# Kernel tuning notes

Measured on AMD Instinct MI355X. Metric: run time of the kernel, lower is better.

Reference implementation:

```python
import jax, jax.numpy as jnp
import numpy as np
from jax import lax

K = 3      # kernel_size
C = 64     # n_feat
B, H, W = 2, 256, 256


def _conv(x, w, b, pad):
    # NCHW conv, stride 1
    out = lax.conv_general_dilated(x, w, (1, 1), [(pad, pad), (pad, pad)],
                                   dimension_numbers=('NCHW', 'OIHW', 'NCHW'))
    return out + b[None, :, None, None]


def _prelu(x, a):
    # nn.PReLU() with a single shared learnable slope (init 0.25)
    return jnp.where(x >= 0, x, a * x)


def setup_inputs():
    key = jax.random.key(0)
    ks = jax.random.split(key, 20)
    s = 0.05
    def w(k, shape):
        return jax.random.normal(k, shape, jnp.float32) * s
    inp = {
        'image': jax.random.normal(ks[0], (B, C, H, W), jnp.float32),
        'guidance': jax.random.normal(ks[1], (B, C, H, W), jnp.float32),
        # self.tensor: 1x1 conv (2C -> C) + PReLU (shared with jbf_conv's act)
        'tensor_w': w(ks[2], (C, 2 * C, 1, 1)),
        'tensor_b': jnp.zeros((C,), jnp.float32),
        'a_jbf': jnp.full((1,), 0.25, jnp.float32),
        'kg_w1': w(ks[3], (C, C, 3, 3)), 'kg_b1': jnp.zeros((C,), jnp.float32),
        'kg_w2': w(ks[4], (C, C, 3, 3)), 'kg_b2': jnp.zeros((C,), jnp.float32),
        'kg_w3': w(ks[5], (C, C, 3, 3)), 'kg_b3': jnp.zeros((C,), jnp.float32),
        'kg_w4': w(ks[6], (C, C, 3, 3)), 'kg_b4': jnp.zeros((C,), jnp.float32),
        'kg_w5': w(ks[7], (K * K * C, C, 1, 1)),
        'kg_b5': jnp.zeros((K * K * C,), jnp.float32),
        'a_kg': jnp.full((1,), 0.25, jnp.float32),
        # jbf_conv: 3x3 C->C, PReLU (shared a_jbf), 3x3 C->C
        'jbf_w1': w(ks[8], (C, C, 3, 3)), 'jbf_b1': jnp.zeros((C,), jnp.float32),
        'jbf_w2': w(ks[9], (C, C, 3, 3)), 'jbf_b2': jnp.zeros((C,), jnp.float32),
    }
    return inp


def reference(image, guidance, tensor_w, tensor_b, a_jbf,
              kg_w1, kg_b1, kg_w2, kg_b2, kg_w3, kg_b3, kg_w4, kg_b4,
              kg_w5, kg_b5, a_kg, jbf_w1, jbf_b1, jbf_w2, jbf_b2):
    b, c, h, w = image.shape
    # fuse target+guidance features
    t = _prelu(_conv(jnp.concatenate([image, guidance], axis=1), tensor_w, tensor_b, 0), a_jbf)
    # concat_kg: predict per-pixel dynamic kernel (b, K*K*c, h, w)
    y = t
    for wt, bs in ((kg_w1, kg_b1), (kg_w2, kg_b2), (kg_w3, kg_b3), (kg_w4, kg_b4)):
        y = _prelu(_conv(y, wt, bs, 1), a_kg)
    bi_kernel = _conv(y, kg_w5, kg_b5, 0)
    # unfold: torch layout is channel-major (c, ki, kj) along dim 1
    p = (K - 1) // 2
    xp = jnp.pad(image, ((0, 0), (0, 0), (p, p), (p, p)))
    taps = [xp[:, :, i:i + h, j:j + w] for i in range(K) for j in range(K)]
    patch = jnp.stack(taps, axis=2).reshape(b, c * K * K, h, w)
    # NOTE: faithful to source -- (c*K*K) flat layout reinterpreted as (K*K, c)
    jbf = (patch * bi_kernel).reshape(b, K * K, c, h, w).sum(axis=1)
    out = _conv(_prelu(_conv(jbf, jbf_w1, jbf_b1, 1), a_jbf), jbf_w2, jbf_b2, 1)
    return out + image
```

## Files before the change

### kernel.cpp

```cpp
#include <hip/hip_runtime.h>

#define HW 65536

typedef __bf16 bf16x8 __attribute__((ext_vector_type(8)));
typedef float f32x16 __attribute__((ext_vector_type(16)));

__device__ inline unsigned short f2bf(float x) {
    union { float f; unsigned u; } v; v.f = x;
    unsigned r = v.u + 0x7FFF + ((v.u >> 16) & 1);
    return (unsigned short)(r >> 16);
}
__device__ inline float bfhi2f(unsigned u) {
    union { unsigned u; float f; } v; v.u = u & 0xffff0000u; return v.f;
}
__device__ inline float bflo2f(unsigned u) {
    union { unsigned u; float f; } v; v.u = u << 16; return v.f;
}

union FragU { uint4 u; bf16x8 v; };
__device__ inline bf16x8 ld_frag(const uint4* p) { FragU t; t.u = *p; return t.v; }

__global__ __launch_bounds__(256) void k_wprep(
    const float* __restrict__ w0, const float* __restrict__ w1,
    const float* __restrict__ w2, const float* __restrict__ w3,
    const float* __restrict__ w4, const float* __restrict__ w5,
    const float* __restrict__ w5c, const float* __restrict__ tw,
    unsigned short* __restrict__ wT)
{
    int y = blockIdx.y;
    unsigned short* o = wT + (size_t)y * 36864;
    if (y < 6) {
        const float* ws_[6] = {w0, w1, w2, w3, w4, w5};
        const float* w = ws_[y];
        for (int e = blockIdx.x * 256 + threadIdx.x; e < 36864; e += gridDim.x * 256) {
            int tap = e >> 12, oc = (e >> 6) & 63, ic = e & 63;
            int igg = ic >> 3, j = ic & 7;
            int dst = ((tap * 8 + igg) * 64 + oc) * 8 + j;
            o[dst] = f2bf(w[(oc * 64 + ic) * 9 + tap]);
        }
    } else if (y == 6) {
        for (int e = blockIdx.x * 256 + threadIdx.x; e < 36864; e += gridDim.x * 256)
            o[e] = f2bf(w5c[e]);
    } else {
        for (int e = blockIdx.x * 256 + threadIdx.x; e < 8192; e += gridDim.x * 256) {
            int oc = e >> 7, ic = e & 127;
            int kg = ic >> 3, j = ic & 7;
            o[((kg * 64 + oc) << 3) + j] = f2bf(tw[e]);
        }
    }
}

__global__ __launch_bounds__(256) void k_tr(
    const float* __restrict__ img, const float* __restrict__ gd,
    unsigned short* __restrict__ imgT, unsigned short* __restrict__ gdT)
{
    __shared__ float sT[64 * 66];
    int tid = threadIdx.x;
    int z = blockIdx.y;
    int b = z & 1;
    const float* src = (z >> 1) ? gd : img;
    unsigned short* dst = (z >> 1) ? gdT : imgT;
    int px0 = blockIdx.x * 64;
    size_t sbase = (size_t)b * 64 * HW + px0;

#pragma unroll
    for (int i = 0; i < 4; ++i) {
        int e = i * 256 + tid;
        int ic = e >> 4, seg = e & 15;
        float4 v = *(const float4*)(src + sbase + (size_t)ic * HW + seg * 4);
        float* p = &sT[ic * 66 + seg * 4];
        ((float2*)p)[0] = make_float2(v.x, v.y);
        ((float2*)p)[1] = make_float2(v.z, v.w);
    }
    __syncthreads();

    size_t dbase = (size_t)b * HW * 64 + (size_t)px0 * 64;
#pragma unroll
    for (int k = 0; k < 2; ++k) {
        int idx = k * 256 + tid;
        int px = idx >> 3, u = idx & 7;
        union { uint4 q; unsigned short h[8]; } o;
#pragma unroll
        for (int j = 0; j < 8; ++j)
            o.h[j] = f2bf(sT[(u * 8 + j) * 66 + px]);
        *(uint4*)(dst + dbase + (size_t)px * 64 + u * 8) = o.q;
    }
}

__global__ __launch_bounds__(256, 4) void k_fusem(
    const unsigned short* __restrict__ imgT, const unsigned short* __restrict__ gdT,
    const unsigned short* __restrict__ wTf, const float* __restrict__ bias,
    const float* __restrict__ a, unsigned short* __restrict__ out)
{
    __shared__ __align__(16) char smem[18688];
    uint4* sX = (uint4*)smem;
    float* sB = (float*)(smem + 18432);
    unsigned short* sT16 = (unsigned short*)smem;

    int tid = threadIdx.x;
    int wv = tid >> 6, lane = tid & 63;
    int half = lane >> 5, l31 = lane & 31;
    int b = blockIdx.z;
    int y0 = blockIdx.y * 8, x0 = blockIdx.x * 16;
    size_t zbase = (size_t)b * HW * 64;
    const uint4* wg = (const uint4*)wTf;

    if (tid < 64) sB[tid] = bias[tid];

    f32x16 acc[2];
#pragma unroll
    for (int i = 0; i < 2; ++i)
#pragma unroll
        for (int r = 0; r < 16; ++r) acc[i][r] = 0.f;

    auto loadX = [&](const unsigned short* src, uint4* rx) {
#pragma unroll
        for (int i = 0; i < 4; ++i) {
            int e = i * 256 + tid;
            int px = e >> 3, ig = e & 7;
            int gy = y0 + (px >> 4), gx = x0 + (px & 15);
            rx[i] = *(const uint4*)(src + zbase + ((size_t)(gy * 256 + gx)) * 64 + ig * 8);
        }
    };
    auto writeX = [&](const uint4* rx) {
#pragma unroll
        for (int i = 0; i < 4; ++i) {
            int e = i * 256 + tid;
            sX[(e >> 3) * 9 + (e & 7)] = rx[i];
        }
    };
    auto compute = [&](int h) {
#pragma unroll
        for (int c = 0; c < 4; ++c) {
            int ig = c * 2 + half;
            int kg = h * 8 + ig;
            bf16x8 a0 = ld_frag(&wg[kg * 64 + l31]);
            bf16x8 a1 = ld_frag(&wg[kg * 64 + 32 + l31]);
            int p0 = wv * 32 + l31;
            bf16x8 b0 = ld_frag(&sX[p0 * 9 + ig]);
            acc[0] = __builtin_amdgcn_mfma_f32_32x32x16_bf16(a0, b0, acc[0], 0, 0, 0);
            acc[1] = __builtin_amdgcn_mfma_f32_32x32x16_bf16(a1, b0, acc[1], 0, 0, 0);
        }
    };

    uint4 rx[4], ry[4];
    loadX(imgT, rx);
    writeX(rx);
    loadX(gdT, ry);
    __syncthreads();
    compute(0);
    __syncthreads();
    writeX(ry);
    __syncthreads();
    compute(1);

    float slope = a[0];
    __syncthreads();
    {
        int px = wv * 32 + l31;
#pragma unroll
        for (int ot = 0; ot < 2; ++ot)
#pragma unroll
            for (int q2 = 0; q2 < 4; ++q2) {
                unsigned short hw[4];
#pragma unroll
                for (int j = 0; j < 4; ++j) {
                    int r = (q2 << 2) | j;
                    int oc = ot * 32 + j + 8 * q2 + 4 * half;
                    float v = acc[ot][r] + sB[oc];
                    v = (v >= 0.f) ? v : slope * v;
                    hw[j] = f2bf(v);
                }
                int unit = ot * 4 + q2;
                int up = unit ^ (px & 7);
                uint2* p = (uint2*)&sT16[px * 64 + up * 8 + half * 4];
                *p = make_uint2((unsigned)hw[0] | ((unsigned)hw[1] << 16),
                                (unsigned)hw[2] | ((unsigned)hw[3] << 16));
            }
    }
    __syncthreads();
#pragma unroll
    for (int k = 0; k < 4; ++k) {
        int idx = k * 256 + tid;
        int row = idx >> 7, rem = idx & 127;
        int col = rem >> 3, u = rem & 7;
        int px = row * 16 + col;
        uint4 v = *(uint4*)&sT16[px * 64 + (u ^ (px & 7)) * 8];
        *(uint4*)(out + zbase + ((size_t)((y0 + row) * 256 + x0 + col)) * 64 + u * 8) = v;
    }
}

#define XU 5

template<int MODE>
__global__ __launch_bounds__(256, 4) void k_conv2x(
    const unsigned short* __restrict__ in,
    const unsigned short* __restrict__ w1T, const unsigned short* __restrict__ w2T,
    const float* __restrict__ b1, const float* __restrict__ b2,
    const float* __restrict__ a, const float* __restrict__ res,
    void* __restrict__ outv)
{
    __shared__ __align__(16) char smem[38912];
    uint4* sIn0 = (uint4*)smem;
    uint4* sIn1 = (uint4*)(smem + 19200);
    float* sB = (float*)(smem + 38400);

    int tid = threadIdx.x;
    int wv = tid >> 6, lane = tid & 63;
    int half = lane >> 5, l31 = lane & 31;
    int b = blockIdx.z;
    int y0 = blockIdx.y * 8, x0 = blockIdx.x * 16;
    const size_t zbase = (size_t)b * HW * 64;
    const uint4* wg1 = (const uint4*)w1T;
    const uint4* wg2 = (const uint4*)w2T;

    if (tid < 64) sB[tid] = b1[tid];
    else if (tid < 128) sB[tid] = b2[tid - 64];

    auto loadIn = [&](int h, uint4* rx) {
#pragma unroll
        for (int i = 0; i < 4; ++i) {
            int e = i * 256 + tid;
            int cell = e >> 2, ig = e & 3;
            int r = cell / 20, c2 = cell - r * 20;
            int gy = y0 - 2 + r, gx = x0 - 2 + c2;
            rx[i] = make_uint4(0, 0, 0, 0);
            if (e < 960 && gy >= 0 && gy < 256 && gx >= 0 && gx < 256)
                rx[i] = *(const uint4*)(in + zbase + ((size_t)(gy * 256 + gx)) * 64 + h * 32 + ig * 8);
        }
    };
    auto writeIn = [&](uint4* s, const uint4* rx) {
#pragma unroll
        for (int i = 0; i < 4; ++i) {
            int e = i * 256 + tid;
            if (e < 960) s[(e >> 2) * XU + (e & 3)] = rx[i];
        }
    };

    const bool two = (wv < 2);
    int cell0 = wv * 32 + l31;
    int ib0 = (cell0 / 18) * 20 + (cell0 % 18);
    int cell1 = (wv + 4) * 32 + l31;
    int cc1 = cell1 < 179 ? cell1 : 179;
    int ib1 = (cc1 / 18) * 20 + (cc1 % 18);

    f32x16 acc1[2][2];
#pragma unroll
    for (int s = 0; s < 2; ++s)
#pragma unroll
        for (int i = 0; i < 2; ++i)
#pragma unroll
            for (int r = 0; r < 16; ++r) acc1[s][i][r] = 0.f;

    auto conv1_h = [&](int h, const uint4* sInp) {
#pragma unroll 1
        for (int dy = 0; dy < 3; ++dy) {
#pragma unroll
            for (int dx = 0; dx < 3; ++dx) {
                int tap = dy * 3 + dx;
                int doff = dy * 20 + dx;
#pragma unroll
                for (int c = 0; c < 2; ++c) {
                    int ig = c * 2 + half;
                    bf16x8 a0 = ld_frag(&wg1[(tap * 8 + h * 4 + ig) * 64 + l31]);
                    bf16x8 a1 = ld_frag(&wg1[(tap * 8 + h * 4 + ig) * 64 + 32 + l31]);
                    bf16x8 bb0 = ld_frag(&sInp[(ib0 + doff) * XU + ig]);
                    acc1[0][0] = __builtin_amdgcn_mfma_f32_32x32x16_bf16(a0, bb0, acc1[0][0], 0, 0, 0);
                    acc1[0][1] = __builtin_amdgcn_mfma_f32_32x32x16_bf16(a1, bb0, acc1[0][1], 0, 0, 0);
                    if (two) {
                        bf16x8 bb1 = ld_frag(&sInp[(ib1 + doff) * XU + ig]);
                        acc1[1][0] = __builtin_amdgcn_mfma_f32_32x32x16_bf16(a0, bb1, acc1[1][0], 0, 0, 0);
                        acc1[1][1] = __builtin_amdgcn_mfma_f32_32x32x16_bf16(a1, bb1, acc1[1][1], 0, 0, 0);
                    }
                }
            }
        }
    };

    uint4 rx[4];
    loadIn(0, rx);
    writeIn(sIn0, rx);
    uint4 ry[4];
    loadIn(1, ry);
    __syncthreads();
    conv1_h(0, sIn0);
    writeIn(sIn1, ry);
    __syncthreads();
    conv1_h(1, sIn1);

    float s1 = a[0];
    __syncthreads();
    unsigned short* sC16 = (unsigned short*)smem;
#pragma unroll
    for (int s = 0; s < 2; ++s) {
        if (s == 1 && !two) break;
        int cell = (wv + s * 4) * 32 + l31;
        if (cell < 180) {
            int orow = cell / 18, ocol = cell - orow * 18;
            int gy = y0 - 1 + orow, gx = x0 - 1 + ocol;
            bool inb = (gy >= 0 && gy < 256 && gx >= 0 && gx < 256);
#pragma unroll
            for (int ot = 0; ot < 2; ++ot)
#pragma unroll
                for (int q2 = 0; q2 < 4; ++q2) {
                    unsigned short hw[4];
#pragma unroll
                    for (int j = 0; j < 4; ++j) {
                        int r = (q2 << 2) | j;
                        int oc = ot * 32 + j + 8 * q2 + 4 * half;
                        float v = acc1[s][ot][r] + sB[oc];
                        v = (v >= 0.f) ? v : s1 * v;
                        if (!inb) v = 0.f;
                        hw[j] = f2bf(v);
                    }
                    int up = (ot * 4 + q2) ^ (cell & 7);
                    *(uint2*)&sC16[cell * 64 + up * 8 + half * 4] =
                        make_uint2((unsigned)hw[0] | ((unsigned)hw[1] << 16),
                                   (unsigned)hw[2] | ((unsigned)hw[3] << 16));
                }
        }
    }
    __syncthreads();

    f32x16 acc2[2];
#pragma unroll
    for (int i = 0; i < 2; ++i)
#pragma unroll
        for (int r = 0; r < 16; ++r) acc2[i][r] = 0.f;

    {
        int p0 = wv * 32 + l31;
        int row = p0 >> 4, col = p0 & 15;
        const uint4* sC4 = (const uint4*)smem;
#pragma unroll 1
        for (int dy = 0; dy < 3; ++dy) {
#pragma unroll
            for (int dx = 0; dx < 3; ++dx) {
                int tap = dy * 3 + dx;
                int cl = (row + dy) * 18 + col + dx;
                int cb = cl * 8, sx = cl & 7;
#pragma unroll
                for (int c = 0; c < 4; ++c) {
                    int ig = c * 2 + half;
                    bf16x8 a0 = ld_frag(&wg2[(tap * 8 + ig) * 64 + l31]);
                    bf16x8 a1 = ld_frag(&wg2[(tap * 8 + ig) * 64 + 32 + l31]);
                    bf16x8 bb = ld_frag(&sC4[cb + (ig ^ sx)]);
                    acc2[0] = __builtin_amdgcn_mfma_f32_32x32x16_bf16(a0, bb, acc2[0], 0, 0, 0);
                    acc2[1] = __builtin_amdgcn_mfma_f32_32x32x16_bf16(a1, bb, acc2[1], 0, 0, 0);
                }
            }
        }
    }

    if (MODE == 0) {
        __syncthreads();
        unsigned short* sT16 = (unsigned short*)smem;
        {
            int px = wv * 32 + l31;
#pragma unroll
            for (int ot = 0; ot < 2; ++ot)
#pragma unroll
                for (int q2 = 0; q2 < 4; ++q2) {
                    unsigned short hw[4];
#pragma unroll
                    for (int j = 0; j < 4; ++j) {
                        int r = (q2 << 2) | j;
                        int oc = ot * 32 + j + 8 * q2 + 4 * half;
                        float v = acc2[ot][r] + sB[64 + oc];
                        v = (v >= 0.f) ? v : s1 * v;
                        hw[j] = f2bf(v);
                    }
                    int unit = ot * 4 + q2;
                    int up = unit ^ (px & 7);
                    uint2* p = (uint2*)&sT16[px * 64 + up * 8 + half * 4];
                    *p = make_uint2((unsigned)hw[0] | ((unsigned)hw[1] << 16),
                                    (unsigned)hw[2] | ((unsigned)hw[3] << 16));
                }
        }
        __syncthreads();
        unsigned short* outT = (unsigned short*)outv;
#pragma unroll
        for (int k = 0; k < 4; ++k) {
            int idx = k * 256 + tid;
            int row = idx >> 7, rem = idx & 127;
            int col = rem >> 3, u = rem & 7;
            int px = row * 16 + col;
            uint4 v = *(uint4*)&sT16[px * 64 + (u ^ (px & 7)) * 8];
            *(uint4*)(outT + zbase + ((size_t)((y0 + row) * 256 + x0 + col)) * 64 + u * 8) = v;
        }
    } else {
        float* outF = (float*)outv;
        int p = wv * 32 + l31;
        int y = y0 + (p >> 4), x = x0 + (p & 15);
        size_t pbase = (size_t)b * 64 * HW + (size_t)y * 256 + x;
#pragma unroll
        for (int ot = 0; ot < 2; ++ot)
#pragma unroll
            for (int r = 0; r < 16; ++r) {
                int oc = ot * 32 + (r & 3) + 8 * (r >> 2) + 4 * half;
                float v = acc2[ot][r] + sB[64 + oc];
                v += res[pbase + (size_t)oc * HW];
                outF[pbase + (size_t)oc * HW] = v;
            }
    }
}

struct OffTab { unsigned v[9][32]; int chlo[9]; };
constexpr OffTab make_tab() {
    OffTab t{};
    for (int kk = 0; kk < 9; ++kk) {
        int chlo = (kk * 64) / 9;
        t.chlo[kk] = chlo;
        for (int ot = 0; ot < 2; ++ot)
            for (int r = 0; r < 16; ++r) {
                int cc0 = ot * 32 + (r & 3) + 8 * (r >> 2);
                int q0 = kk * 64 + cc0, q1 = q0 + 4;
                int o0 = (q0 / 9 - chlo) * 360 + (q0 % 9 / 3) * 40 + (q0 % 9 % 3);
                int o1 = (q1 / 9 - chlo) * 360 + (q1 % 9 / 3) * 40 + (q1 % 9 % 3);
                t.v[kk][ot * 16 + r] = (unsigned)o0 | ((unsigned)o1 << 16);
            }
    }
    return t;
}
__constant__ OffTab kOff = make_tab();

__global__ __launch_bounds__(256, 2) void k_jbfm(
    const unsigned short* __restrict__ y4, const float* __restrict__ img,
    const unsigned short* __restrict__ w5T, const float* __restrict__ b5,
    unsigned short* __restrict__ out)
{
    __shared__ __align__(16) char smem[78592];
    uint4* sY = (uint4*)smem;
    float* sB5 = (float*)(smem + 76288);
    unsigned short* sT16 = (unsigned short*)smem;

    int tid = threadIdx.x;
    int wv = tid >> 6, lane = tid & 63;
    int half = lane >> 5, l31 = lane & 31;
    int b = blockIdx.z;
    int y0 = blockIdx.y * 8, x0 = blockIdx.x * 32;
    size_t zbase = (size_t)b * HW * 64;
    size_t ibase = (size_t)b * 64 * HW;

    int p_off[3], p_dst[3];
    bool p_a[3], p_b[3], p_act[3];
#pragma unroll
    for (int i = 0; i < 3; ++i) {
        int e = i * 256 + tid;
        bool act = e < 720;
        int ch = e / 90, rem = e - ch * 90;
        int rp = rem / 10, seg = rem - rp * 10;
        int gy = y0 + rp - 1;
        int gxb = x0 - 4 + seg * 4;
        bool xok = (gxb >= 0 && gxb < 256);
        p_act[i] = act;
        p_a[i] = act && xok && gy >= 0 && gy < 256;
        p_b[i] = act && xok && (gy + 1) < 256;
        p_off[i] = ch * HW + gy * 256 + gxb;
        p_dst[i] = ch * 360 + rp * 40 + seg * 4;
    }

#pragma unroll
    for (int i = 0; i < 8; ++i) {
        int e = i * 256 + tid;
        int px = e >> 3, ig = e & 7;
        int gy = y0 + (px >> 5), gx = x0 + (px & 31);
        sY[px * 9 + ig] = *(const uint4*)(y4 + zbase + ((size_t)(gy * 256 + gx)) * 64 + ig * 8);
    }
    for (int e = tid; e < 576; e += 256) sB5[e] = b5[e];

    {
        uint4* sW50 = (uint4*)(smem + 36864);
        unsigned* sP0 = (unsigned*)(smem + 53248);
#pragma unroll
        for (int u = 0; u < 2; ++u) {
            int uu = u * 256 + tid;
            int cc = uu & 63, ig = uu >> 6;
            sW50[uu] = ((const uint4*)w5T)[cc * 8 + ig];
        }
        const float* rp0 = img + ibase;
#pragma unroll
        for (int i = 0; i < 3; ++i) {
            float4 fa = make_float4(0, 0, 0, 0), fb = make_float4(0, 0, 0, 0);
            if (p_a[i]) fa = *(const float4*)(rp0 + p_off[i]);
            if (p_b[i]) fb = *(const float4*)(rp0 + p_off[i] + 256);
            if (p_act[i]) {
                uint4 pk;
                pk.x = (unsigned)f2bf(fa.x) | ((unsigned)f2bf(fb.x) << 16);
                pk.y = (unsigned)f2bf(fa.y) | ((unsigned)f2bf(fb.y) << 16);
                pk.z = (unsigned)f2bf(fa.z) | ((unsigned)f2bf(fb.z) << 16);
                pk.w = (unsigned)f2bf(fa.w) | ((unsigned)f2bf(fb.w) << 16);
                *(uint4*)&sP0[p_dst[i]] = pk;
            }
        }
    }

    float jb[2][2][16];
#pragma unroll
    for (int i = 0; i < 2; ++i)
#pragma unroll
        for (int j = 0; j < 2; ++j)
#pragma unroll
            for (int r = 0; r < 16; ++r) jb[i][j][r] = 0.f;

    __syncthreads();

#pragma unroll 1
    for (int kk = 0; kk < 9; ++kk) {
        const int cur = kk & 1;
        const uint4* sW5c = (const uint4*)(smem + 36864 + cur * 8192);
        const unsigned* sPc = (const unsigned*)(smem + 53248 + cur * 11520);

        uint4 wpre0, wpre1;
        float4 pfa[3], pfb[3];
        if (kk < 8) {
            const int nk = kk + 1;
            const int chlo_n = kOff.chlo[nk];
            {
                int cc = tid & 63, ig = tid >> 6;
                wpre0 = ((const uint4*)w5T)[(nk * 64 + cc) * 8 + ig];
                int uu = 256 + tid;
                int cc1 = uu & 63, ig1 = uu >> 6;
                wpre1 = ((const uint4*)w5T)[(nk * 64 + cc1) * 8 + ig1];
            }
            const float* rp0 = img + ibase + (size_t)chlo_n * HW;
#pragma unroll
            for (int i = 0; i < 3; ++i) {
                pfa[i] = make_float4(0, 0, 0, 0);
                pfb[i] = make_float4(0, 0, 0, 0);
                if (p_a[i]) pfa[i] = *(const float4*)(rp0 + p_off[i]);
                if (p_b[i]) pfb[i] = *(const float4*)(rp0 + p_off[i] + 256);
            }
        }

        f32x16 acc[2][2];
#pragma unroll
        for (int ot = 0; ot < 2; ++ot)
#pragma unroll
            for (int r = 0; r < 16; ++r) {
                int cc0 = ot * 32 + (r & 3) + 8 * (r >> 2);
                float bv = sB5[kk * 64 + cc0 + 4 * half];
                acc[ot][0][r] = bv;
                acc[ot][1][r] = bv;
            }

#pragma unroll
        for (int c = 0; c < 4; ++c) {
            int ig = c * 2 + half;
            bf16x8 a0 = ld_frag(&sW5c[ig * 64 + l31]);
            bf16x8 a1 = ld_frag(&sW5c[ig * 64 + 32 + l31]);
            int p0 = wv * 64 + l31;
            bf16x8 b0 = ld_frag(&sY[p0 * 9 + ig]);
            bf16x8 b1 = ld_frag(&sY[(p0 + 32) * 9 + ig]);
            acc[0][0] = __builtin_amdgcn_mfma_f32_32x32x16_bf16(a0, b0, acc[0][0], 0, 0, 0);
            acc[0][1] = __builtin_amdgcn_mfma_f32_32x32x16_bf16(a0, b1, acc[0][1], 0, 0, 0);
            acc[1][0] = __builtin_amdgcn_mfma_f32_32x32x16_bf16(a1, b0, acc[1][0], 0, 0, 0);
            acc[1][1] = __builtin_amdgcn_mfma_f32_32x32x16_bf16(a1, b1, acc[1][1], 0, 0, 0);
        }

        {
            const unsigned* basep = sPc + wv * 80 + l31 + 3;
            const unsigned* tab = kOff.v[kk];
#pragma unroll
            for (int ot = 0; ot < 2; ++ot)
#pragma unroll
                for (int r = 0; r < 16; ++r) {
                    unsigned oo = tab[ot * 16 + r];
                    unsigned o0 = oo & 0xffffu, o1 = oo >> 16;
                    unsigned pv = basep[half ? o1 : o0];
                    jb[ot][0][r] = fmaf(acc[ot][0][r], bflo2f(pv), jb[ot][0][r]);
                    jb[ot][1][r] = fmaf(acc[ot][1][r], bfhi2f(pv), jb[ot][1][r]);
                }
        }

        if (kk < 8) {
            uint4* sW5n = (uint4*)(smem + 36864 + (cur ^ 1) * 8192);
            unsigned* sPn = (unsigned*)(smem + 53248 + (cur ^ 1) * 11520);
            sW5n[tid] = wpre0;
            sW5n[256 + tid] = wpre1;
#pragma unroll
            for (int i = 0; i < 3; ++i) {
                if (p_act[i]) {
                    uint4 pk;
                    pk.x = (unsigned)f2bf(pfa[i].x) | ((unsigned)f2bf(pfb[i].x) << 16);
                    pk.y = (unsigned)f2bf(pfa[i].y) | ((unsigned)f2bf(pfb[i].y) << 16);
                    pk.z = (unsigned)f2bf(pfa[i].z) | ((unsigned)f2bf(pfb[i].z) << 16);
                    pk.w = (unsigned)f2bf(pfa[i].w) | ((unsigned)f2bf(pfb[i].w) << 16);
                    *(uint4*)&sPn[p_dst[i]] = pk;
                }
            }
        }
        __syncthreads();
    }

#pragma unroll
    for (int ot = 0; ot < 2; ++ot)
#pragma unroll
        for (int pt = 0; pt < 2; ++pt) {
            int px = wv * 64 + pt * 32 + l31;
#pragma unroll
            for (int q2 = 0; q2 < 4; ++q2) {
                unsigned short hw[4];
#pragma unroll
                for (int j = 0; j < 4; ++j) {
                    int r = (q2 << 2) | j;
                    hw[j] = f2bf(jb[ot][pt][r]);
                }
                int unit = ot * 4 + q2;
                int up = unit ^ (px & 7);
                uint2* p = (uint2*)&sT16[px * 64 + up * 8 + half * 4];
                *p = make_uint2((unsigned)hw[0] | ((unsigned)hw[1] << 16),
                                (unsigned)hw[2] | ((unsigned)hw[3] << 16));
            }
        }
    __syncthreads();
#pragma unroll
    for (int k = 0; k < 8; ++k) {
        int col = tid >> 3, u = tid & 7;
        int px = k * 32 + col;
        uint4 v = *(uint4*)&sT16[px * 64 + (u ^ (px & 7)) * 8];
        *(uint4*)(out + zbase + ((size_t)((y0 + k) * 256 + x0 + col)) * 64 + u * 8) = v;
    }
}

extern "C" void kernel_launch(void* const* d_in, const int* in_sizes, int n_in,
                              void* d_out, int out_size, void* d_ws, size_t ws_size,
                              hipStream_t stream) {
    const float* img  = (const float*)d_in[0];
    const float* gd   = (const float*)d_in[1];
    const float* tw   = (const float*)d_in[2];
    const float* tb   = (const float*)d_in[3];
    const float* ajbf = (const float*)d_in[4];
    const float* kw1  = (const float*)d_in[5];
    const float* kb1  = (const float*)d_in[6];
    const float* kw2  = (const float*)d_in[7];
    const float* kb2  = (const float*)d_in[8];
    const float* kw3  = (const float*)d_in[9];
    const float* kb3  = (const float*)d_in[10];
    const float* kw4  = (const float*)d_in[11];
    const float* kb4  = (const float*)d_in[12];
    const float* kw5  = (const float*)d_in[13];
    const float* kb5  = (const float*)d_in[14];
    const float* akg  = (const float*)d_in[15];
    const float* jw1  = (const float*)d_in[16];
    const float* jb1  = (const float*)d_in[17];
    const float* jw2  = (const float*)d_in[18];
    const float* jb2  = (const float*)d_in[19];
    float* out  = (float*)d_out;

    const size_t TEN = (size_t)2 * HW * 64;
    unsigned short* bufA = (unsigned short*)d_ws;
    unsigned short* imgT = bufA + TEN;
    unsigned short* gdT  = imgT + TEN;
    unsigned short* wT   = gdT + TEN;
    unsigned short* bufB = (unsigned short*)d_out;
    unsigned short* bufC = gdT;

    dim3 gs(16, 32, 2);
    dim3 gw(8, 32, 2);

    k_tr<<<dim3(1024, 4), 256, 0, stream>>>(img, gd, imgT, gdT);
    k_wprep<<<dim3(4, 8), 256, 0, stream>>>(kw1, kw2, kw3, kw4, jw1, jw2, kw5, tw, wT);

    k_fusem<<<gs, 256, 0, stream>>>(imgT, gdT, wT + (size_t)7 * 36864, tb, ajbf, bufA);

    k_conv2x<0><<<gs, 256, 0, stream>>>(bufA, wT + (size_t)0 * 36864, wT + (size_t)1 * 36864,
                                        kb1, kb2, akg, nullptr, bufB);
    k_conv2x<0><<<gs, 256, 0, stream>>>(bufB, wT + (size_t)2 * 36864, wT + (size_t)3 * 36864,
                                        kb3, kb4, akg, nullptr, bufA);

    k_jbfm<<<gw, 256, 0, stream>>>(bufA, img, wT + (size_t)6 * 36864, kb5, bufC);

    k_conv2x<2><<<gs, 256, 0, stream>>>(bufC, wT + (size_t)4 * 36864, wT + (size_t)5 * 36864,
                                        jb1, jb2, ajbf, img, out);
}
```

Measured before the change: 314.3 us.

## Repartition conv2x MFMA work across waves by output-channel half and pixel group

Each wave in the fused double 3x3 conv now owns one 32-channel half of the output and a group of pixels (3 tiles for conv1, 2 for conv2), instead of all 64 channels for a subset of pixels. This removes the imbalance in conv1, where only two of the four waves handled a second pixel tile. Each wave now loads one weight fragment per step instead of two but reads more input fragments from shared memory. The tap loops are also fully unrolled, which adds register pressure under the launch bound of 4 blocks.

```diff
diff --git a/kernel.cpp b/kernel.cpp
--- a/kernel.cpp
+++ b/kernel.cpp
@@ -208,6 +208,7 @@
     int tid = threadIdx.x;
     int wv = tid >> 6, lane = tid & 63;
     int half = lane >> 5, l31 = lane & 31;
+    int w2 = wv >> 1, g = wv & 1;
     int b = blockIdx.z;
     int y0 = blockIdx.y * 8, x0 = blockIdx.x * 16;
     const size_t zbase = (size_t)b * HW * 64;
@@ -225,7 +226,8 @@
             int r = cell / 20, c2 = cell - r * 20;
             int gy = y0 - 2 + r, gx = x0 - 2 + c2;
             rx[i] = make_uint4(0, 0, 0, 0);
-            if (e < 960 && gy >= 0 && gy < 256 && gx >= 0 && gx < 256)
+            bool act = (i < 3) || (e < 960);
+            if (act && gy >= 0 && gy < 256 && gx >= 0 && gx < 256)
                 rx[i] = *(const uint4*)(in + zbase + ((size_t)(gy * 256 + gx)) * 64 + h * 32 + ig * 8);
         }
     };
@@ -233,27 +235,27 @@
 #pragma unroll
         for (int i = 0; i < 4; ++i) {
             int e = i * 256 + tid;
-            if (e < 960) s[(e >> 2) * XU + (e & 3)] = rx[i];
+            if (i < 3 || e < 960) s[(e >> 2) * XU + (e & 3)] = rx[i];
         }
     };
 
-    const bool two = (wv < 2);
-    int cell0 = wv * 32 + l31;
-    int ib0 = (cell0 / 18) * 20 + (cell0 % 18);
-    int cell1 = (wv + 4) * 32 + l31;
-    int cc1 = cell1 < 179 ? cell1 : 179;
-    int ib1 = (cc1 / 18) * 20 + (cc1 % 18);
-
-    f32x16 acc1[2][2];
-#pragma unroll
-    for (int s = 0; s < 2; ++s)
-#pragma unroll
-        for (int i = 0; i < 2; ++i)
-#pragma unroll
-            for (int r = 0; r < 16; ++r) acc1[s][i][r] = 0.f;
+    int cellv[3], ibv[3];
+#pragma unroll
+    for (int s = 0; s < 3; ++s) {
+        int c = g * 96 + s * 32 + l31;
+        cellv[s] = c;
+        int cc = c < 180 ? c : 179;
+        ibv[s] = (cc / 18) * 20 + (cc % 18);
+    }
+
+    f32x16 acc1[3];
+#pragma unroll
+    for (int s = 0; s < 3; ++s)
+#pragma unroll
+        for (int r = 0; r < 16; ++r) acc1[s][r] = 0.f;
 
     auto conv1_h = [&](int h, const uint4* sInp) {
-#pragma unroll 1
+#pragma unroll
         for (int dy = 0; dy < 3; ++dy) {
 #pragma unroll
             for (int dx = 0; dx < 3; ++dx) {
@@ -262,15 +264,11 @@
 #pragma unroll
                 for (int c = 0; c < 2; ++c) {
                     int ig = c * 2 + half;
-                    bf16x8 a0 = ld_frag(&wg1[(tap * 8 + h * 4 + ig) * 64 + l31]);
-                    bf16x8 a1 = ld_frag(&wg1[(tap * 8 + h * 4 + ig) * 64 + 32 + l31]);
-                    bf16x8 bb0 = ld_frag(&sInp[(ib0 + doff) * XU + ig]);
-                    acc1[0][0] = __builtin_amdgcn_mfma_f32_32x32x16_bf16(a0, bb0, acc1[0][0], 0, 0, 0);
-                    acc1[0][1] = __builtin_amdgcn_mfma_f32_32x32x16_bf16(a1, bb0, acc1[0][1], 0, 0, 0);
-                    if (two) {
-                        bf16x8 bb1 = ld_frag(&sInp[(ib1 + doff) * XU + ig]);
-                        acc1[1][0] = __builtin_amdgcn_mfma_f32_32x32x16_bf16(a0, bb1, acc1[1][0], 0, 0, 0);
-                        acc1[1][1] = __builtin_amdgcn_mfma_f32_32x32x16_bf16(a1, bb1, acc1[1][1], 0, 0, 0);
+                    bf16x8 af = ld_frag(&wg1[(tap * 8 + h * 4 + ig) * 64 + w2 * 32 + l31]);
+#pragma unroll
+                    for (int s = 0; s < 3; ++s) {
+                        bf16x8 bb = ld_frag(&sInp[(ibv[s] + doff) * XU + ig]);
+                        acc1[s] = __builtin_amdgcn_mfma_f32_32x32x16_bf16(af, bb, acc1[s], 0, 0, 0);
                     }
                 }
             }
@@ -292,61 +290,62 @@
     __syncthreads();
     unsigned short* sC16 = (unsigned short*)smem;
 #pragma unroll
-    for (int s = 0; s < 2; ++s) {
-        if (s == 1 && !two) break;
-        int cell = (wv + s * 4) * 32 + l31;
+    for (int s = 0; s < 3; ++s) {
+        int cell = cellv[s];
         if (cell < 180) {
             int orow = cell / 18, ocol = cell - orow * 18;
             int gy = y0 - 1 + orow, gx = x0 - 1 + ocol;
             bool inb = (gy >= 0 && gy < 256 && gx >= 0 && gx < 256);
 #pragma unroll
-            for (int ot = 0; ot < 2; ++ot)
-#pragma unroll
-                for (int q2 = 0; q2 < 4; ++q2) {
-                    unsigned short hw[4];
-#pragma unroll
-                    for (int j = 0; j < 4; ++j) {
-                        int r = (q2 << 2) | j;
-                        int oc = ot * 32 + j + 8 * q2 + 4 * half;
-                        float v = acc1[s][ot][r] + sB[oc];
-                        v = (v >= 0.f) ? v : s1 * v;
-                        if (!inb) v = 0.f;
-                        hw[j] = f2bf(v);
-                    }
-                    int up = (ot * 4 + q2) ^ (cell & 7);
-                    *(uint2*)&sC16[cell * 64 + up * 8 + half * 4] =
-                        make_uint2((unsigned)hw[0] | ((unsigned)hw[1] << 16),
-                                   (unsigned)hw[2] | ((unsigned)hw[3] << 16));
-                }
+            for (int q2 = 0; q2 < 4; ++q2) {
+                unsigned short hw[4];
+#pragma unroll
+                for (int j = 0; j < 4; ++j) {
+                    int r = (q2 << 2) | j;
+                    int oc = w2 * 32 + j + 8 * q2 + 4 * half;
+                    float v = acc1[s][r] + sB[oc];
+                    v = (v >= 0.f) ? v : s1 * v;
+                    if (!inb) v = 0.f;
+                    hw[j] = f2bf(v);
+                }
+                int up = (w2 * 4 + q2) ^ (cell & 7);
+                *(uint2*)&sC16[cell * 64 + up * 8 + half * 4] =
+                    make_uint2((unsigned)hw[0] | ((unsigned)hw[1] << 16),
+                               (unsigned)hw[2] | ((unsigned)hw[3] << 16));
+            }
         }
     }
     __syncthreads();
 
     f32x16 acc2[2];
 #pragma unroll
-    for (int i = 0; i < 2; ++i)
-#pragma unroll
-        for (int r = 0; r < 16; ++r) acc2[i][r] = 0.f;
-
+    for (int s = 0; s < 2; ++s)
+#pragma unroll
+        for (int r = 0; r < 16; ++r) acc2[s][r] = 0.f;
+
+    int rowS[2], colS[2];
+#pragma unroll
+    for (int s = 0; s < 2; ++s) {
+        int px = g * 64 + s * 32 + l31;
+        rowS[s] = px >> 4; colS[s] = px & 15;
+    }
     {
-        int p0 = wv * 32 + l31;
-        int row = p0 >> 4, col = p0 & 15;
         const uint4* sC4 = (const uint4*)smem;
-#pragma unroll 1
+#pragma unroll
         for (int dy = 0; dy < 3; ++dy) {
 #pragma unroll
             for (int dx = 0; dx < 3; ++dx) {
                 int tap = dy * 3 + dx;
-                int cl = (row + dy) * 18 + col + dx;
-                int cb = cl * 8, sx = cl & 7;
 #pragma unroll
                 for (int c = 0; c < 4; ++c) {
                     int ig = c * 2 + half;
-                    bf16x8 a0 = ld_frag(&wg2[(tap * 8 + ig) * 64 + l31]);
-                    bf16x8 a1 = ld_frag(&wg2[(tap * 8 + ig) * 64 + 32 + l31]);
-                    bf16x8 bb = ld_frag(&sC4[cb + (ig ^ sx)]);
-                    acc2[0] = __builtin_amdgcn_mfma_f32_32x32x16_bf16(a0, bb, acc2[0], 0, 0, 0);
-                    acc2[1] = __builtin_amdgcn_mfma_f32_32x32x16_bf16(a1, bb, acc2[1], 0, 0, 0);
+                    bf16x8 af = ld_frag(&wg2[(tap * 8 + ig) * 64 + w2 * 32 + l31]);
+#pragma unroll
+                    for (int s = 0; s < 2; ++s) {
+                        int cl = (rowS[s] + dy) * 18 + colS[s] + dx;
+                        bf16x8 bb = ld_frag(&sC4[cl * 8 + (ig ^ (cl & 7))]);
+                        acc2[s] = __builtin_amdgcn_mfma_f32_32x32x16_bf16(af, bb, acc2[s], 0, 0, 0);
+                    }
                 }
             }
         }
@@ -355,27 +354,25 @@
     if (MODE == 0) {
         __syncthreads();
         unsigned short* sT16 = (unsigned short*)smem;
-        {
-            int px = wv * 32 + l31;
-#pragma unroll
-            for (int ot = 0; ot < 2; ++ot)
-#pragma unroll
-                for (int q2 = 0; q2 < 4; ++q2) {
-                    unsigned short hw[4];
-#pragma unroll
-                    for (int j = 0; j < 4; ++j) {
-                        int r = (q2 << 2) | j;
-                        int oc = ot * 32 + j + 8 * q2 + 4 * half;
-                        float v = acc2[ot][r] + sB[64 + oc];
-                        v = (v >= 0.f) ? v : s1 * v;
-                        hw[j] = f2bf(v);
-                    }
-                    int unit = ot * 4 + q2;
-                    int up = unit ^ (px & 7);
-                    uint2* p = (uint2*)&sT16[px * 64 + up * 8 + half * 4];
-                    *p = make_uint2((unsigned)hw[0] | ((unsigned)hw[1] << 16),
-                                    (unsigned)hw[2] | ((unsigned)hw[3] << 16));
-                }
+#pragma unroll
+        for (int s = 0; s < 2; ++s) {
+            int px = g * 64 + s * 32 + l31;
+#pragma unroll
+            for (int q2 = 0; q2 < 4; ++q2) {
+                unsigned short hw[4];
+#pragma unroll
+                for (int j = 0; j < 4; ++j) {
+                    int r = (q2 << 2) | j;
+                    int oc = w2 * 32 + j + 8 * q2 + 4 * half;
+                    float v = acc2[s][r] + sB[64 + oc];
+                    v = (v >= 0.f) ? v : s1 * v;
+                    hw[j] = f2bf(v);
+                }
+                int up = (w2 * 4 + q2) ^ (px & 7);
+                uint2* p = (uint2*)&sT16[px * 64 + up * 8 + half * 4];
+                *p = make_uint2((unsigned)hw[0] | ((unsigned)hw[1] << 16),
+                                (unsigned)hw[2] | ((unsigned)hw[3] << 16));
+            }
         }
         __syncthreads();
         unsigned short* outT = (unsigned short*)outv;
@@ -390,18 +387,19 @@
         }
     } else {
         float* outF = (float*)outv;
-        int p = wv * 32 + l31;
-        int y = y0 + (p >> 4), x = x0 + (p & 15);
-        size_t pbase = (size_t)b * 64 * HW + (size_t)y * 256 + x;
-#pragma unroll
-        for (int ot = 0; ot < 2; ++ot)
+#pragma unroll
+        for (int s = 0; s < 2; ++s) {
+            int px = g * 64 + s * 32 + l31;
+            int y = y0 + (px >> 4), x = x0 + (px & 15);
+            size_t pbase = (size_t)b * 64 * HW + (size_t)y * 256 + x;
 #pragma unroll
             for (int r = 0; r < 16; ++r) {
-                int oc = ot * 32 + (r & 3) + 8 * (r >> 2) + 4 * half;
-                float v = acc2[ot][r] + sB[64 + oc];
+                int oc = w2 * 32 + (r & 3) + 8 * (r >> 2) + 4 * half;
+                float v = acc2[s][r] + sB[64 + oc];
                 v += res[pbase + (size_t)oc * HW];
                 outF[pbase + (size_t)oc * HW] = v;
             }
+        }
     }
 }
 
```

Result: no change. 311.5 us (-0.9%).
